# Optimization experiments

Measured on AMD Instinct MI355X. Metric: run time of the kernel, lower is better.

The kernel has to match this reference:

```python
import jax, jax.numpy as jnp
import numpy as np

HIDDEN = 1024
N_HEAD = 16
N_KV_HEAD = 4
HEAD_DIM = HIDDEN // N_HEAD  # 64


def setup_inputs() -> dict:
    key = jax.random.key(0)
    ks = jax.random.split(key, 9)
    s = 0.02
    kv_dim = N_KV_HEAD * HEAD_DIM
    return {
        "X": jax.random.normal(ks[0], (2, 2048, HIDDEN), dtype=jnp.float32),
        "Wq": jax.random.normal(ks[1], (HIDDEN, HIDDEN), dtype=jnp.float32) * s,
        "bq": jnp.zeros((HIDDEN,), dtype=jnp.float32),
        "Wk": jax.random.normal(ks[2], (HIDDEN, kv_dim), dtype=jnp.float32) * s,
        "bk": jnp.zeros((kv_dim,), dtype=jnp.float32),
        "Wv": jax.random.normal(ks[3], (HIDDEN, kv_dim), dtype=jnp.float32) * s,
        "bv": jnp.zeros((kv_dim,), dtype=jnp.float32),
        "Wo": jax.random.normal(ks[4], (HIDDEN, HIDDEN), dtype=jnp.float32) * s,
        "bo": jnp.zeros((HIDDEN,), dtype=jnp.float32),
    }


def reference(X, Wq, bq, Wk, bk, Wv, bv, Wo, bo):
    B, S, _ = X.shape
    rep = N_HEAD // N_KV_HEAD
    # projections
    q = (X @ Wq + bq).reshape(B, S, N_HEAD, HEAD_DIM).transpose(0, 2, 1, 3)      # [B,H,S,D]
    k = (X @ Wk + bk).reshape(B, S, N_KV_HEAD, HEAD_DIM).transpose(0, 2, 1, 3)   # [B,Hkv,S,D]
    v = (X @ Wv + bv).reshape(B, S, N_KV_HEAD, HEAD_DIM).transpose(0, 2, 1, 3)
    # repeat_interleave KV heads to full head count (faithful to original)
    k = jnp.repeat(k, rep, axis=1)  # [B,H,S,D]
    v = jnp.repeat(v, rep, axis=1)
    scale = 1.0 / jnp.sqrt(jnp.float32(HEAD_DIM))
    scores = jnp.einsum("bhqd,bhkd->bhqk", q, k) * scale  # [B,H,S,S]
    weights = jax.nn.softmax(scores, axis=-1)
    out = jnp.einsum("bhqk,bhkd->bhqd", weights, v)       # [B,H,S,D]
    out = out.transpose(0, 2, 1, 3).reshape(B, S, HIDDEN)
    return out @ Wo + bo
```

## Files before the change

kernel.cpp:

```cpp
#include <hip/hip_runtime.h>
#include <hip/hip_bf16.h>

#define HIDDEN 1024
#define NHEAD 16
#define NKV 4
#define HDIM 64
#define KVDIM 256
#define SEQ 2048
#define BATCH 2
#define NQKV 1536

typedef __attribute__((ext_vector_type(4)))  float f32x4;
typedef __attribute__((ext_vector_type(16))) float f32x16;
typedef __attribute__((ext_vector_type(8)))  short s16x8;
typedef __attribute__((ext_vector_type(4)))  short s16x4;

#if defined(__has_builtin)
#if __has_builtin(__builtin_amdgcn_exp2f)
#define EXP2F(x) __builtin_amdgcn_exp2f(x)
#else
#define EXP2F(x) exp2f(x)
#endif
#else
#define EXP2F(x) exp2f(x)
#endif

static __device__ __forceinline__ ushort f2bf(float f) {
    union { __hip_bfloat16 b; ushort u; } cv; cv.b = __float2bfloat16(f); return cv.u;
}
static __device__ __forceinline__ unsigned pack_rh2(float a, float b) {
    unsigned ua = __float_as_uint(a) + 0x8000u;
    unsigned ub = __float_as_uint(b) + 0x8000u;
    return (ua >> 16) | (ub & 0xFFFF0000u);
}
static __device__ __forceinline__ void async16(const void* g, void* l) {
    __builtin_amdgcn_global_load_lds((__attribute__((address_space(1))) void*)g,
                                     (__attribute__((address_space(3))) void*)l, 16, 0, 0);
}

__global__ __launch_bounds__(256)
void cvt_x(const float* __restrict__ in, ushort* __restrict__ out)
{
    int i = blockIdx.x * 256 + threadIdx.x;
    float4 v = ((const float4*)in)[i];
    ushort4 o;
    o.x = f2bf(v.x); o.y = f2bf(v.y); o.z = f2bf(v.z); o.w = f2bf(v.w);
    ((ushort4*)out)[i] = o;
}

__global__ __launch_bounds__(256)
void wtrans_qkv(const float* __restrict__ Wq, const float* __restrict__ Wk,
                const float* __restrict__ Wv, ushort* __restrict__ T)
{
    __shared__ float Tl[64][65];
    const int bx = blockIdx.x, k0 = blockIdx.y * 64;
    const float* W; int N, n0, roff;
    if (bx < 16)      { W = Wq; N = 1024; n0 = bx * 64;        roff = 0; }
    else if (bx < 20) { W = Wk; N = 256;  n0 = (bx - 16) * 64; roff = 1024; }
    else              { W = Wv; N = 256;  n0 = (bx - 20) * 64; roff = 1280; }
    const int tid = threadIdx.x;
#pragma unroll
    for (int it = 0; it < 4; it++) {
        int idx = tid + it * 256;
        int kk = idx >> 4, n4 = (idx & 15) * 4;
        float4 v = *(const float4*)(W + (size_t)(k0 + kk) * N + n0 + n4);
        Tl[kk][n4 + 0] = v.x; Tl[kk][n4 + 1] = v.y;
        Tl[kk][n4 + 2] = v.z; Tl[kk][n4 + 3] = v.w;
    }
    __syncthreads();
#pragma unroll
    for (int it = 0; it < 4; it++) {
        int idx = tid + it * 256;
        int n = idx >> 4, k4 = (idx & 15) * 4;
        ushort4 h4;
        h4.x = f2bf(Tl[k4 + 0][n]); h4.y = f2bf(Tl[k4 + 1][n]);
        h4.z = f2bf(Tl[k4 + 2][n]); h4.w = f2bf(Tl[k4 + 3][n]);
        *(ushort4*)(T + (size_t)(roff + n0 + n) * HIDDEN + k0 + k4) = h4;
    }
}

__global__ __launch_bounds__(256)
void wtrans_one(const float* __restrict__ W, ushort* __restrict__ T,
                int N, int K)
{
    __shared__ float Tl[64][65];
    const int n0 = blockIdx.x * 64, k0 = blockIdx.y * 64;
    const int tid = threadIdx.x;
#pragma unroll
    for (int it = 0; it < 4; it++) {
        int idx = tid + it * 256;
        int kk = idx >> 4, n4 = (idx & 15) * 4;
        float4 v = *(const float4*)(W + (size_t)(k0 + kk) * N + n0 + n4);
        Tl[kk][n4 + 0] = v.x; Tl[kk][n4 + 1] = v.y;
        Tl[kk][n4 + 2] = v.z; Tl[kk][n4 + 3] = v.w;
    }
    __syncthreads();
#pragma unroll
    for (int it = 0; it < 4; it++) {
        int idx = tid + it * 256;
        int n = idx >> 4, k4 = (idx & 15) * 4;
        ushort4 h4;
        h4.x = f2bf(Tl[k4 + 0][n]); h4.y = f2bf(Tl[k4 + 1][n]);
        h4.z = f2bf(Tl[k4 + 2][n]); h4.w = f2bf(Tl[k4 + 3][n]);
        *(ushort4*)(T + (size_t)(n0 + n) * K + k0 + k4) = h4;
    }
}

template <int MODE>
__global__ __launch_bounds__(256)
void gemm_bf(const ushort* __restrict__ A, const ushort* __restrict__ Bt,
             const float* __restrict__ b0, const float* __restrict__ b1,
             const float* __restrict__ b2, void* __restrict__ Cout,
             int M, int N, int K)
{
    __shared__ __align__(16) ushort Ah[128 * 32];
    __shared__ __align__(16) ushort Bh[128 * 32];

    const int tid = threadIdx.x;
    const int lane = tid & 63, wv = tid >> 6;
    const int wr = wv >> 1, wc = wv & 1;
    const int m = lane & 15, c = lane >> 4;
    const int row0 = blockIdx.y * 128, col0 = blockIdx.x * 128;

    const ushort* gA[2]; const ushort* gB[2]; int ldsO[2];
#pragma unroll
    for (int it = 0; it < 2; it++) {
        int idx = it * 256 + tid;
        gA[it] = A  + (size_t)(row0 + (idx >> 2)) * K + (idx & 3) * 8;
        gB[it] = Bt + (size_t)(col0 + (idx >> 2)) * K + (idx & 3) * 8;
        ldsO[it] = idx * 8;
    }

    f32x4 acc[4][4];
#pragma unroll
    for (int t = 0; t < 4; t++)
#pragma unroll
        for (int u = 0; u < 4; u++) acc[t][u] = (f32x4){0.f, 0.f, 0.f, 0.f};

    for (int k0 = 0; k0 < K; k0 += 32) {
        __syncthreads();
#pragma unroll
        for (int it = 0; it < 2; it++) {
            async16(gA[it] + k0, Ah + ldsO[it]);
            async16(gB[it] + k0, Bh + ldsO[it]);
        }
        __syncthreads();

        s16x8 ah[4], bh[4];
#pragma unroll
        for (int t = 0; t < 4; t++)
            ah[t] = *(const s16x8*)&Ah[(wr * 64 + t * 16 + m) * 32 + c * 8];
#pragma unroll
        for (int u = 0; u < 4; u++)
            bh[u] = *(const s16x8*)&Bh[(wc * 64 + u * 16 + m) * 32 + c * 8];
#pragma unroll
        for (int t = 0; t < 4; t++)
#pragma unroll
            for (int u = 0; u < 4; u++)
                acc[t][u] = __builtin_amdgcn_mfma_f32_16x16x32_bf16(ah[t], bh[u], acc[t][u], 0, 0, 0);
    }

    const int orow = row0 + wr * 64 + 4 * c;
    const int ocol = col0 + wc * 64 + m;
    if (MODE == 0) {
        ushort* Cb = (ushort*)Cout;
#pragma unroll
        for (int u = 0; u < 4; u++) {
            int n = ocol + 16 * u;
            float bias, scl;
            if (n < 1024)      { bias = b0[n];        scl = 0.18033688f; }
            else if (n < 1280) { bias = b1[n - 1024]; scl = 1.0f; }
            else               { bias = b2[n - 1280]; scl = 1.0f; }
#pragma unroll
            for (int t = 0; t < 4; t++)
#pragma unroll
                for (int r = 0; r < 4; r++)
                    Cb[(size_t)(orow + 16 * t + r) * N + n] = f2bf((acc[t][u][r] + bias) * scl);
        }
    } else {
        float* Cf = (float*)Cout;
#pragma unroll
        for (int u = 0; u < 4; u++) {
            int n = ocol + 16 * u;
            float bias = b0[n];
#pragma unroll
            for (int t = 0; t < 4; t++)
#pragma unroll
                for (int r = 0; r < 4; r++)
                    Cf[(size_t)(orow + 16 * t + r) * N + n] = acc[t][u][r] + bias;
        }
    }
}

__global__ __launch_bounds__(256)
void kvpack(const ushort* __restrict__ QKV, ushort* __restrict__ Kf,
            ushort* __restrict__ Vf)
{
    __shared__ __align__(16) ushort Kt[64][72];
    __shared__ __align__(16) ushort Vt[64][72];
    const int kt = blockIdx.x, hk = blockIdx.y, b = blockIdx.z;
    const int tid = threadIdx.x;

#pragma unroll
    for (int it = 0; it < 2; it++) {
        int idx = tid + it * 256;
        int r = idx >> 3, c8 = (idx & 7) * 8;
        const ushort* src = QKV + (size_t)(b * SEQ + kt * 64 + r) * NQKV + hk * HDIM + c8;
        *(s16x8*)&Kt[r][c8] = *(const s16x8*)(src + 1024);
        *(s16x8*)&Vt[r][c8] = *(const s16x8*)(src + 1280);
    }
    __syncthreads();

#pragma unroll
    for (int it = 0; it < 2; it++) {
        int idx = tid + it * 256;
        int t32 = idx >> 8, kc = (idx >> 6) & 3, lane = idx & 63;
        int n32 = lane & 31, h5 = lane >> 5;
        s16x8 fr = *(const s16x8*)&Kt[t32 * 32 + n32][kc * 16 + h5 * 8];
        size_t flat = ((size_t)(((b * NKV + hk) * 64 + kt * 2 + t32) * 4 + kc) * 64 + lane) * 8;
        *(s16x8*)(Kf + flat) = fr;
    }
#pragma unroll
    for (int it = 0; it < 2; it++) {
        int idx = tid + it * 256;
        int kcdn = idx >> 6, lane = idx & 63;
        int kc = kcdn >> 1, dn = kcdn & 1;
        int n32 = lane & 31, h5 = lane >> 5;
        s16x8 fr;
#pragma unroll
        for (int j = 0; j < 8; j++)
            fr[j] = (short)Vt[kc * 16 + h5 * 8 + j][dn * 32 + n32];
        size_t flat = ((size_t)(((b * NKV + hk) * 32 + kt) * 8 + kc * 2 + dn) * 64 + lane) * 8;
        *(s16x8*)(Vf + flat) = fr;
    }
}

__global__ __launch_bounds__(512, 2)
void attn_mfma7(const ushort* __restrict__ QKV, const ushort* __restrict__ Kf,
                const ushort* __restrict__ Vf, ushort* __restrict__ Chi)
{
    __shared__ __align__(16) ushort Ps[8][32][68];
    float* OLb = (float*)&Ps[0][0][0];
    float* LLb = (float*)((char*)&Ps[0][0][0] + 33024);

    const int tid = threadIdx.x, w = tid >> 6, lane = tid & 63;
    const int g = w >> 2, ws_ = w & 3;
    const int n32 = lane & 31, h5 = lane >> 5;
    const int h = blockIdx.y, b = blockIdx.z, hk = h >> 2;
    const int q0 = blockIdx.x * 64 + g * 32;

    const ushort* qrow = QKV + (size_t)(b * SEQ + q0 + n32) * NQKV + h * HDIM + h5 * 8;
    s16x8 aq[4];
#pragma unroll
    for (int kc = 0; kc < 4; kc++) aq[kc] = *(const s16x8*)(qrow + kc * 16);

    f32x16 accO[2], accl;
#pragma unroll
    for (int j = 0; j < 16; j++) { accO[0][j] = 0.f; accO[1][j] = 0.f; accl[j] = 0.f; }

    s16x8 ones;
#pragma unroll
    for (int j = 0; j < 8; j++) ones[j] = (short)0x3F80;

    const ushort* kf0 = Kf + (size_t)(b * NKV + hk) * (64 * 4 * 64 * 8) + (size_t)lane * 8;
    const ushort* vf0 = Vf + (size_t)(b * NKV + hk) * (32 * 8 * 64 * 8) + (size_t)lane * 8;

    s16x8 kreg[8], vreg[8];

#define LOAD_K(kt_) do {                                                      \
    _Pragma("unroll")                                                         \
    for (int kn = 0; kn < 2; kn++)                                            \
        _Pragma("unroll")                                                     \
        for (int kc = 0; kc < 4; kc++)                                        \
            kreg[kn * 4 + kc] =                                               \
                *(const s16x8*)(kf0 + (size_t)(((kt_) * 2 + kn) * 4 + kc) * 512); \
} while (0)

#define LOAD_V(kt_) do {                                                      \
    _Pragma("unroll")                                                         \
    for (int kc = 0; kc < 4; kc++)                                            \
        _Pragma("unroll")                                                     \
        for (int dn = 0; dn < 2; dn++)                                        \
            vreg[kc * 2 + dn] =                                               \
                *(const s16x8*)(vf0 + (size_t)((kt_) * 8 + kc * 2 + dn) * 512); \
} while (0)

#define QK_EXP_STORE() do {                                                   \
    _Pragma("unroll")                                                         \
    for (int kn = 0; kn < 2; kn++) {                                          \
        f32x16 S;                                                             \
        _Pragma("unroll")                                                     \
        for (int j = 0; j < 16; j++) S[j] = 0.f;                              \
        _Pragma("unroll")                                                     \
        for (int kc = 0; kc < 4; kc++)                                        \
            S = __builtin_amdgcn_mfma_f32_32x32x16_bf16(kreg[kn * 4 + kc],    \
                    aq[kc], S, 0, 0, 0);                                      \
        float p[16];                                                          \
        _Pragma("unroll")                                                     \
        for (int reg = 0; reg < 16; reg++) p[reg] = EXP2F(S[reg]);            \
        _Pragma("unroll")                                                     \
        for (int t = 0; t < 4; t++) {                                         \
            uint2 pk;                                                         \
            pk.x = pack_rh2(p[4 * t + 0], p[4 * t + 1]);                      \
            pk.y = pack_rh2(p[4 * t + 2], p[4 * t + 3]);                      \
            *(uint2*)&Ps[w][n32][kn * 32 + 8 * t + 4 * h5] = pk;              \
        }                                                                     \
    }                                                                         \
} while (0)

#define PV_STEP() do {                                                        \
    s16x8 pa[4];                                                              \
    _Pragma("unroll")                                                         \
    for (int kc = 0; kc < 4; kc++) {                                          \
        s16x4 lo4 = *(const s16x4*)&Ps[w][n32][kc * 16 + h5 * 8];             \
        s16x4 hi4 = *(const s16x4*)&Ps[w][n32][kc * 16 + h5 * 8 + 4];         \
        pa[kc] = __builtin_shufflevector(lo4, hi4, 0, 1, 2, 3, 4, 5, 6, 7);   \
    }                                                                         \
    _Pragma("unroll")                                                         \
    for (int kc = 0; kc < 4; kc++) {                                          \
        accl = __builtin_amdgcn_mfma_f32_32x32x16_bf16(pa[kc], ones, accl, 0, 0, 0); \
        _Pragma("unroll")                                                     \
        for (int dn = 0; dn < 2; dn++)                                        \
            accO[dn] = __builtin_amdgcn_mfma_f32_32x32x16_bf16(pa[kc],        \
                           vreg[kc * 2 + dn], accO[dn], 0, 0, 0);             \
    }                                                                         \
} while (0)

    LOAD_K(ws_);
    QK_EXP_STORE();

    for (int i = 1; i < 8; i++) {
        const int ktc = ws_ + 4 * i;
        LOAD_V(ktc - 4);
        LOAD_K(ktc);
        PV_STEP();
        QK_EXP_STORE();
    }

    LOAD_V(ws_ + 28);
    PV_STEP();

#undef LOAD_K
#undef LOAD_V
#undef QK_EXP_STORE
#undef PV_STEP

    __syncthreads();

    const int qq = tid >> 4;
    const int d0 = (tid & 15) * 4;
#pragma unroll
    for (int phase = 0; phase < 2; phase++) {
        if (g == phase) {
#pragma unroll
            for (int reg = 0; reg < 16; reg++) {
                int q = (reg & 3) + 8 * (reg >> 2) + 4 * h5;
                OLb[(ws_ * 32 + q) * 64 + n32]      = accO[0][reg];
                OLb[(ws_ * 32 + q) * 64 + 32 + n32] = accO[1][reg];
                if (n32 == 0) LLb[ws_ * 32 + q] = accl[reg];
            }
        }
        __syncthreads();
        {
            float lsum = LLb[qq] + LLb[32 + qq] + LLb[64 + qq] + LLb[96 + qq];
            float inv = 1.f / lsum;
            ushort4 hs;
            float o0 = (OLb[(0 * 32 + qq) * 64 + d0 + 0] + OLb[(1 * 32 + qq) * 64 + d0 + 0] +
                        OLb[(2 * 32 + qq) * 64 + d0 + 0] + OLb[(3 * 32 + qq) * 64 + d0 + 0]) * inv;
            float o1 = (OLb[(0 * 32 + qq) * 64 + d0 + 1] + OLb[(1 * 32 + qq) * 64 + d0 + 1] +
                        OLb[(2 * 32 + qq) * 64 + d0 + 1] + OLb[(3 * 32 + qq) * 64 + d0 + 1]) * inv;
            float o2 = (OLb[(0 * 32 + qq) * 64 + d0 + 2] + OLb[(1 * 32 + qq) * 64 + d0 + 2] +
                        OLb[(2 * 32 + qq) * 64 + d0 + 2] + OLb[(3 * 32 + qq) * 64 + d0 + 2]) * inv;
            float o3 = (OLb[(0 * 32 + qq) * 64 + d0 + 3] + OLb[(1 * 32 + qq) * 64 + d0 + 3] +
                        OLb[(2 * 32 + qq) * 64 + d0 + 3] + OLb[(3 * 32 + qq) * 64 + d0 + 3]) * inv;
            hs.x = f2bf(o0); hs.y = f2bf(o1); hs.z = f2bf(o2); hs.w = f2bf(o3);
            size_t off = (size_t)(b * SEQ + blockIdx.x * 64 + phase * 32 + qq) * HIDDEN
                       + h * HDIM + d0;
            *(ushort4*)(Chi + off) = hs;
        }
        __syncthreads();
    }
}

extern "C" void kernel_launch(void* const* d_in, const int* in_sizes, int n_in,
                              void* d_out, int out_size, void* d_ws, size_t ws_size,
                              hipStream_t stream)
{
    const float* X  = (const float*)d_in[0];
    const float* Wq = (const float*)d_in[1];
    const float* bq = (const float*)d_in[2];
    const float* Wk = (const float*)d_in[3];
    const float* bk = (const float*)d_in[4];
    const float* Wv = (const float*)d_in[5];
    const float* bv = (const float*)d_in[6];
    const float* Wo = (const float*)d_in[7];
    const float* bo = (const float*)d_in[8];
    float* out = (float*)d_out;

    const int M = BATCH * SEQ;
    char* ws = (char*)d_ws;
    ushort* Xb    = (ushort*)(ws);
    ushort* Ctx   = (ushort*)(ws + (8u  << 20));
    ushort* QKVb  = (ushort*)(ws + (16u << 20));
    ushort* Wqkvt = (ushort*)(ws + (28u << 20));
    ushort* Wot   = (ushort*)(ws + (31u << 20));
    ushort* Kf    = (ushort*)(ws + (33u << 20));
    ushort* Vf    = (ushort*)(ws + (35u << 20));

    cvt_x<<<dim3(M * HIDDEN / 4 / 256), 256, 0, stream>>>(X, Xb);
    wtrans_qkv<<<dim3(24, 16), 256, 0, stream>>>(Wq, Wk, Wv, Wqkvt);
    wtrans_one<<<dim3(16, 16), 256, 0, stream>>>(Wo, Wot, 1024, HIDDEN);

    gemm_bf<0><<<dim3(NQKV / 128, M / 128), 256, 0, stream>>>(
        Xb, Wqkvt, bq, bk, bv, (void*)QKVb, M, NQKV, HIDDEN);

    kvpack<<<dim3(SEQ / 64, NKV, BATCH), 256, 0, stream>>>(QKVb, Kf, Vf);

    attn_mfma7<<<dim3(SEQ / 64, NHEAD, BATCH), 512, 0, stream>>>(QKVb, Kf, Vf, Ctx);

    gemm_bf<1><<<dim3(HIDDEN / 128, M / 128), 256, 0, stream>>>(
        Ctx, Wot, bo, nullptr, nullptr, (void*)out, M, HIDDEN, HIDDEN);
}
```

Measured before the change: 199.6 us.

## Merge prep kernels, widen QKV GEMM tile, add MFMA priority hints in attention

Fuses the X conversion and both weight transposes into a single prep launch to cut launch overhead. Templates the GEMM on tile width and thread count so the QKV projection uses 128x192 tiles with 6 waves, giving 8x32=256 blocks that match the CU count. Wraps the attention MFMA sequences in s_setprio to favour matrix issue over other waves. This trades some generality in the GEMM load mapping (a predicated tail) for the fewer launches and better CU fill.

After: 212.5 us. 6.4% more time.

```diff
diff --git a/kernel.cpp b/kernel.cpp
--- a/kernel.cpp
+++ b/kernel.cpp
@@ -39,26 +39,37 @@
 }
 
 __global__ __launch_bounds__(256)
-void cvt_x(const float* __restrict__ in, ushort* __restrict__ out)
-{
-    int i = blockIdx.x * 256 + threadIdx.x;
-    float4 v = ((const float4*)in)[i];
-    ushort4 o;
-    o.x = f2bf(v.x); o.y = f2bf(v.y); o.z = f2bf(v.z); o.w = f2bf(v.w);
-    ((ushort4*)out)[i] = o;
-}
-
-__global__ __launch_bounds__(256)
-void wtrans_qkv(const float* __restrict__ Wq, const float* __restrict__ Wk,
-                const float* __restrict__ Wv, ushort* __restrict__ T)
+void prep(const float* __restrict__ X, ushort* __restrict__ Xb,
+          const float* __restrict__ Wq, const float* __restrict__ Wk,
+          const float* __restrict__ Wv, ushort* __restrict__ Tqkv,
+          const float* __restrict__ Wo, ushort* __restrict__ Two)
 {
     __shared__ float Tl[64][65];
-    const int bx = blockIdx.x, k0 = blockIdx.y * 64;
-    const float* W; int N, n0, roff;
-    if (bx < 16)      { W = Wq; N = 1024; n0 = bx * 64;        roff = 0; }
-    else if (bx < 20) { W = Wk; N = 256;  n0 = (bx - 16) * 64; roff = 1024; }
-    else              { W = Wv; N = 256;  n0 = (bx - 20) * 64; roff = 1280; }
-    const int tid = threadIdx.x;
+    const int bid = blockIdx.x, tid = threadIdx.x;
+
+    if (bid < 4096) {
+        int i = bid * 256 + tid;
+        float4 v = ((const float4*)X)[i];
+        ushort4 o;
+        o.x = f2bf(v.x); o.y = f2bf(v.y); o.z = f2bf(v.z); o.w = f2bf(v.w);
+        ((ushort4*)Xb)[i] = o;
+        return;
+    }
+
+    const float* W; ushort* T; int N, n0, k0, roff;
+    if (bid < 4096 + 384) {
+        int wq = bid - 4096;
+        int bx = wq % 24; k0 = (wq / 24) * 64;
+        T = Tqkv;
+        if (bx < 16)      { W = Wq; N = 1024; n0 = bx * 64;        roff = 0; }
+        else if (bx < 20) { W = Wk; N = 256;  n0 = (bx - 16) * 64; roff = 1024; }
+        else              { W = Wv; N = 256;  n0 = (bx - 20) * 64; roff = 1280; }
+    } else {
+        int wo = bid - 4480;
+        int bx = wo % 16; k0 = (wo / 16) * 64;
+        W = Wo; T = Two; N = 1024; n0 = bx * 64; roff = 0;
+    }
+
 #pragma unroll
     for (int it = 0; it < 4; it++) {
         int idx = tid + it * 256;
@@ -79,56 +90,42 @@
     }
 }
 
-__global__ __launch_bounds__(256)
-void wtrans_one(const float* __restrict__ W, ushort* __restrict__ T,
-                int N, int K)
-{
-    __shared__ float Tl[64][65];
-    const int n0 = blockIdx.x * 64, k0 = blockIdx.y * 64;
-    const int tid = threadIdx.x;
-#pragma unroll
-    for (int it = 0; it < 4; it++) {
-        int idx = tid + it * 256;
-        int kk = idx >> 4, n4 = (idx & 15) * 4;
-        float4 v = *(const float4*)(W + (size_t)(k0 + kk) * N + n0 + n4);
-        Tl[kk][n4 + 0] = v.x; Tl[kk][n4 + 1] = v.y;
-        Tl[kk][n4 + 2] = v.z; Tl[kk][n4 + 3] = v.w;
-    }
-    __syncthreads();
-#pragma unroll
-    for (int it = 0; it < 4; it++) {
-        int idx = tid + it * 256;
-        int n = idx >> 4, k4 = (idx & 15) * 4;
-        ushort4 h4;
-        h4.x = f2bf(Tl[k4 + 0][n]); h4.y = f2bf(Tl[k4 + 1][n]);
-        h4.z = f2bf(Tl[k4 + 2][n]); h4.w = f2bf(Tl[k4 + 3][n]);
-        *(ushort4*)(T + (size_t)(n0 + n) * K + k0 + k4) = h4;
-    }
-}
-
-template <int MODE>
-__global__ __launch_bounds__(256)
+template <int MODE, int BN, int NT>
+__global__ __launch_bounds__(NT)
 void gemm_bf(const ushort* __restrict__ A, const ushort* __restrict__ Bt,
              const float* __restrict__ b0, const float* __restrict__ b1,
              const float* __restrict__ b2, void* __restrict__ Cout,
              int M, int N, int K)
 {
-    __shared__ __align__(16) ushort Ah[128 * 32];
-    __shared__ __align__(16) ushort Bh[128 * 32];
+    constexpr int BM = 128;
+    constexpr int NWC = BN / 64;
+    constexpr int SA = BM * 4;
+    constexpr int SB = BN * 4;
+    constexpr int TOT = SA + SB;
+    constexpr int ITERS = (TOT + NT - 1) / NT;
+
+    __shared__ __align__(16) ushort Ah[BM * 32];
+    __shared__ __align__(16) ushort Bh[BN * 32];
 
     const int tid = threadIdx.x;
     const int lane = tid & 63, wv = tid >> 6;
-    const int wr = wv >> 1, wc = wv & 1;
+    const int wr = wv / NWC, wc = wv % NWC;
     const int m = lane & 15, c = lane >> 4;
-    const int row0 = blockIdx.y * 128, col0 = blockIdx.x * 128;
-
-    const ushort* gA[2]; const ushort* gB[2]; int ldsO[2];
-#pragma unroll
-    for (int it = 0; it < 2; it++) {
-        int idx = it * 256 + tid;
-        gA[it] = A  + (size_t)(row0 + (idx >> 2)) * K + (idx & 3) * 8;
-        gB[it] = Bt + (size_t)(col0 + (idx >> 2)) * K + (idx & 3) * 8;
-        ldsO[it] = idx * 8;
+    const int row0 = blockIdx.y * BM, col0 = blockIdx.x * BN;
+
+    const ushort* gsrc[ITERS]; ushort* ldst[ITERS]; bool val[ITERS];
+#pragma unroll
+    for (int it = 0; it < ITERS; it++) {
+        int s = it * NT + tid;
+        val[it] = ((it + 1) * NT <= TOT) || (tid < TOT - it * NT);
+        if (s < SA) {
+            gsrc[it] = A + (size_t)(row0 + (s >> 2)) * K + (s & 3) * 8;
+            ldst[it] = Ah + s * 8;
+        } else {
+            int sb = s - SA; if (sb >= SB) sb = 0;
+            gsrc[it] = Bt + (size_t)(col0 + (sb >> 2)) * K + (sb & 3) * 8;
+            ldst[it] = Bh + sb * 8;
+        }
     }
 
     f32x4 acc[4][4];
@@ -140,10 +137,8 @@
     for (int k0 = 0; k0 < K; k0 += 32) {
         __syncthreads();
 #pragma unroll
-        for (int it = 0; it < 2; it++) {
-            async16(gA[it] + k0, Ah + ldsO[it]);
-            async16(gB[it] + k0, Bh + ldsO[it]);
-        }
+        for (int it = 0; it < ITERS; it++)
+            if (val[it]) async16(gsrc[it] + k0, ldst[it]);
         __syncthreads();
 
         s16x8 ah[4], bh[4];
@@ -236,7 +231,7 @@
 }
 
 __global__ __launch_bounds__(512, 2)
-void attn_mfma7(const ushort* __restrict__ QKV, const ushort* __restrict__ Kf,
+void attn_mfma8(const ushort* __restrict__ QKV, const ushort* __restrict__ Kf,
                 const ushort* __restrict__ Vf, ushort* __restrict__ Chi)
 {
     __shared__ __align__(16) ushort Ps[8][32][68];
@@ -291,10 +286,12 @@
         f32x16 S;                                                             \
         _Pragma("unroll")                                                     \
         for (int j = 0; j < 16; j++) S[j] = 0.f;                              \
+        __builtin_amdgcn_s_setprio(1);                                        \
         _Pragma("unroll")                                                     \
         for (int kc = 0; kc < 4; kc++)                                        \
             S = __builtin_amdgcn_mfma_f32_32x32x16_bf16(kreg[kn * 4 + kc],    \
                     aq[kc], S, 0, 0, 0);                                      \
+        __builtin_amdgcn_s_setprio(0);                                        \
         float p[16];                                                          \
         _Pragma("unroll")                                                     \
         for (int reg = 0; reg < 16; reg++) p[reg] = EXP2F(S[reg]);            \
@@ -316,6 +313,7 @@
         s16x4 hi4 = *(const s16x4*)&Ps[w][n32][kc * 16 + h5 * 8 + 4];         \
         pa[kc] = __builtin_shufflevector(lo4, hi4, 0, 1, 2, 3, 4, 5, 6, 7);   \
     }                                                                         \
+    __builtin_amdgcn_s_setprio(1);                                            \
     _Pragma("unroll")                                                         \
     for (int kc = 0; kc < 4; kc++) {                                          \
         accl = __builtin_amdgcn_mfma_f32_32x32x16_bf16(pa[kc], ones, accl, 0, 0, 0); \
@@ -324,6 +322,7 @@
             accO[dn] = __builtin_amdgcn_mfma_f32_32x32x16_bf16(pa[kc],        \
                            vreg[kc * 2 + dn], accO[dn], 0, 0, 0);             \
     }                                                                         \
+    __builtin_amdgcn_s_setprio(0);                                            \
 } while (0)
 
     LOAD_K(ws_);
@@ -407,17 +406,15 @@
     ushort* Kf    = (ushort*)(ws + (33u << 20));
     ushort* Vf    = (ushort*)(ws + (35u << 20));
 
-    cvt_x<<<dim3(M * HIDDEN / 4 / 256), 256, 0, stream>>>(X, Xb);
-    wtrans_qkv<<<dim3(24, 16), 256, 0, stream>>>(Wq, Wk, Wv, Wqkvt);
-    wtrans_one<<<dim3(16, 16), 256, 0, stream>>>(Wo, Wot, 1024, HIDDEN);
-
-    gemm_bf<0><<<dim3(NQKV / 128, M / 128), 256, 0, stream>>>(
+    prep<<<dim3(4736), 256, 0, stream>>>(X, Xb, Wq, Wk, Wv, Wqkvt, Wo, Wot);
+
+    gemm_bf<0, 192, 384><<<dim3(NQKV / 192, M / 128), 384, 0, stream>>>(
         Xb, Wqkvt, bq, bk, bv, (void*)QKVb, M, NQKV, HIDDEN);
 
     kvpack<<<dim3(SEQ / 64, NKV, BATCH), 256, 0, stream>>>(QKVb, Kf, Vf);
 
-    attn_mfma7<<<dim3(SEQ / 64, NHEAD, BATCH), 512, 0, stream>>>(QKVb, Kf, Vf, Ctx);
-
-    gemm_bf<1><<<dim3(HIDDEN / 128, M / 128), 256, 0, stream>>>(
+    attn_mfma8<<<dim3(SEQ / 64, NHEAD, BATCH), 512, 0, stream>>>(QKVb, Kf, Vf, Ctx);
+
+    gemm_bf<1, 128, 256><<<dim3(HIDDEN / 128, M / 128), 256, 0, stream>>>(
         Ctx, Wot, bo, nullptr, nullptr, (void*)out, M, HIDDEN, HIDDEN);
 }
```
